# Optimization experiments

Measured on AMD Instinct MI355X. Metric: run time of the kernel, lower is better.

## Reference

```python
import jax, jax.numpy as jnp
import numpy as np
from jax import lax

QMAX = 15.0   # 4-bit unsigned activation levels
BN_EPS = 1e-5


def _binarize_irnet(w):
    # IR-Net style 1-bit weights: per-output-channel normalize, sign, rescale by mean |w|.
    mu = jnp.mean(w, axis=(1, 2, 3), keepdims=True)
    std = jnp.std(w, axis=(1, 2, 3), keepdims=True)
    wn = (w - mu) / (std + 1e-5)
    scale = jnp.mean(jnp.abs(wn), axis=(1, 2, 3), keepdims=True)
    wc = jnp.clip(wn, -1.0, 1.0)
    # STE: forward=sign(wn), backward=hardtanh passthrough
    bw = wc + lax.stop_gradient(jnp.sign(wn) - wc)
    return bw * scale


def _lsq_act_4bit(x, alpha):
    # LSQ unsigned 4-bit: clamp(x/alpha, 0, 15), round with STE, rescale.
    xs = jnp.clip(x / alpha, 0.0, QMAX)
    xq = xs + lax.stop_gradient(jnp.round(xs) - xs)
    return xq * alpha


def _qconv_bn_relu(x, w, alpha, g, b, m, v, stride):
    xq = _lsq_act_4bit(x, alpha)
    bw = _binarize_irnet(w)
    y = lax.conv_general_dilated(
        xq, bw, window_strides=(stride, stride), padding=((1, 1), (1, 1)),
        dimension_numbers=('NCHW', 'OIHW', 'NCHW'))
    inv = g / jnp.sqrt(v + BN_EPS)
    y = y * inv[None, :, None, None] + (b - m * inv)[None, :, None, None]
    return jax.nn.relu(y)


def setup_inputs() -> dict:
    key = jax.random.key(0)
    ks = jax.random.split(key, 3)
    B, C, H, W = 32, 256, 56, 56
    x = jax.random.normal(ks[0], (B, C, H, W), dtype=jnp.float32)
    w1 = jax.random.normal(ks[1], (C, C, 3, 3), dtype=jnp.float32) * 0.05
    w2 = jax.random.normal(ks[2], (C, C, 3, 3), dtype=jnp.float32) * 0.05
    ones = jnp.ones((C,), jnp.float32)
    zeros = jnp.zeros((C,), jnp.float32)
    return {
        'x': x,
        'w1': w1, 'alpha1': jnp.float32(0.1), 'g1': ones, 'b1': zeros, 'm1': zeros, 'v1': ones,
        'w2': w2, 'alpha2': jnp.float32(0.1), 'g2': ones, 'b2': zeros, 'm2': zeros, 'v2': ones,
    }


def reference(x, w1, alpha1, g1, b1, m1, v1, w2, alpha2, g2, b2, m2, v2):
    stride = 1
    h = _qconv_bn_relu(x, w1, alpha1, g1, b1, m1, v1, stride)
    out = _qconv_bn_relu(h, w2, alpha2, g2, b2, m2, v2, 1)
    return out
```

## Files before the change

### kernel.cpp

```cpp
#include <hip/hip_runtime.h>
#include <math.h>

typedef int v4i __attribute__((ext_vector_type(4)));
typedef int v16i __attribute__((ext_vector_type(16)));
typedef unsigned long long u64;

#define Bn 32
#define Cc 256
#define Hh 56
#define Ww 56
#define RSTR (34 * 256)
#define ACT_LDS (6 * RSTR)
#define NSTG (6 * 34 * 16)

__device__ __forceinline__ float block_sum(float v, float* red) {
#pragma unroll
    for (int off = 32; off > 0; off >>= 1) v += __shfl_down(v, off, 64);
    const int wv = threadIdx.x >> 6;
    __syncthreads();
    if ((threadIdx.x & 63) == 0) red[wv] = v;
    __syncthreads();
    return red[0] + red[1] + red[2] + red[3];
}

__global__ __launch_bounds__(256) void k_binpack(const float* __restrict__ w,
                                                 signed char* __restrict__ wf,
                                                 float* __restrict__ wsc) {
    __shared__ float red[4];
    const int o = blockIdx.x;
    const float* wo = w + (size_t)o * 2304;
    const int t = threadIdx.x;
    float v[9];
    float s = 0.f, s2 = 0.f;
#pragma unroll
    for (int i = 0; i < 9; ++i) {
        v[i] = wo[t * 9 + i];
        s += v[i];
        s2 += v[i] * v[i];
    }
    s = block_sum(s, red);
    s2 = block_sum(s2, red);
    const float mu = s * (1.f / 2304.f);
    const float sd = sqrtf(fmaxf(s2 * (1.f / 2304.f) - mu * mu, 0.f));
    float sa = 0.f;
#pragma unroll
    for (int i = 0; i < 9; ++i) sa += fabsf(v[i] - mu);
    sa = block_sum(sa, red);
    if (t == 0) wsc[o] = (sa * (1.f / 2304.f)) / (sd + 1e-5f);
    const int c = t, c32 = c >> 5, hf = (c >> 4) & 1, j = c & 15;
    const int lane = (hf << 5) | (o & 31), octile = o >> 5;
#pragma unroll
    for (int tap = 0; tap < 9; ++tap) {
        const float d = v[tap] - mu;
        const signed char sg = (d > 0.f) ? 1 : ((d < 0.f) ? -1 : 0);
        wf[(size_t)(((tap * 8 + c32) * 8 + octile) * 64 + lane) * 16 + j] = sg;
    }
}

__global__ void k_prep(const float* __restrict__ g1, const float* __restrict__ b1,
                       const float* __restrict__ m1, const float* __restrict__ v1,
                       const float* __restrict__ g2, const float* __restrict__ b2,
                       const float* __restrict__ m2, const float* __restrict__ v2,
                       const float* __restrict__ a1p, const float* __restrict__ a2p,
                       const float* __restrict__ ws1, const float* __restrict__ ws2,
                       float* __restrict__ ep) {
    const int i = threadIdx.x;
    const float i1 = g1[i] / sqrtf(v1[i] + 1e-5f);
    const float i2 = g2[i] / sqrtf(v2[i] + 1e-5f);
    ep[i] = a1p[0] * ws1[i] * i1;
    ep[256 + i] = b1[i] - m1[i] * i1;
    ep[512 + i] = a2p[0] * ws2[i] * i2;
    ep[768 + i] = b2[i] - m2[i] * i2;
}

__global__ __launch_bounds__(256) void k_quant_nhwc(const float* __restrict__ x,
                                                    unsigned char* __restrict__ xq,
                                                    const float* __restrict__ ap) {
    __shared__ unsigned char q[3584];
    const int bid = blockIdx.x;
    const int cg = bid & 3;
    const int h = (bid >> 2) % Hh;
    const int n = bid / (4 * Hh);
    const float a = ap[0];
    const int c0 = cg * 64;
    for (int i = threadIdx.x; i < 3584; i += 256) {
        const int cl = i / 56;
        const int w = i - cl * 56;
        const float v = x[(((size_t)n * Cc + c0 + cl) * Hh + h) * Ww + w];
        const float xs = fminf(fmaxf(v / a, 0.f), 15.f);
        q[w * 64 + (((cl >> 2) ^ (w & 15)) << 2) + (cl & 3)] = (unsigned char)(int)rintf(xs);
    }
    __syncthreads();
    const unsigned int* q32 = (const unsigned int*)q;
    unsigned int* dst = (unsigned int*)xq + ((size_t)(n * Hh + h) * Ww) * 32;
    for (int j = threadIdx.x; j < 448; j += 256) {
        const int w = j >> 3, g8l = (j >> 1) & 3, hf = j & 1;
        const unsigned int lo = q32[w * 16 + ((g8l * 4 + hf) ^ (w & 15))];
        const unsigned int hi = q32[w * 16 + ((g8l * 4 + 2 + hf) ^ (w & 15))];
        dst[w * 32 + (cg * 4 + g8l) * 2 + hf] = lo | (hi << 4);
    }
}

template <bool QOUT>
__global__ __launch_bounds__(256, 3) void k_conv(const unsigned char* __restrict__ xin,
                                                 const signed char* __restrict__ wf,
                                                 const float* __restrict__ ep,
                                                 const float* __restrict__ a2p,
                                                 unsigned char* __restrict__ hq,
                                                 float* __restrict__ yout) {
    __shared__ __align__(16) unsigned char sm[ACT_LDS];
    const int bid = blockIdx.x;
    const int oh = bid & 1;
    const int mh = (bid >> 1) & 1;
    const int hb = (bid >> 2) % 14;
    const int n = (bid >> 2) / 14;
    const int h0 = hb * 4;
    const int mbase = mh * 32;
    const int tid = threadIdx.x;
    const int boff = bid & 7;

    {
        u64 tmp[13];
#pragma unroll
        for (int k = 0; k < 13; ++k) {
            int u = tid + (k << 8);
            u = u > (NSTG - 1) ? (NSTG - 1) : u;
            const int r = u / 544;
            const int rem = u - r * 544;
            const int col = rem >> 4;
            const int t8 = rem & 15;
            int y = h0 - 1 + r;
            int xi = mbase - 1 + col;
            y = y < 0 ? 0 : (y > 55 ? 55 : y);
            xi = xi < 0 ? 0 : (xi > 55 ? 55 : xi);
            tmp[k] = *(const u64*)(xin + ((((size_t)n * Hh + y) * Ww + xi) << 7) + (t8 << 3));
        }
#pragma unroll
        for (int k = 0; k < 13; ++k) {
            const int u = tid + (k << 8);
            if (u < NSTG) {
                const int r = u / 544;
                const int rem = u - r * 544;
                const int col = rem >> 4;
                const int t8 = rem & 15;
                const int y = h0 - 1 + r;
                const int xi = mbase - 1 + col;
                const u64 p = ((unsigned)y < 56u && (unsigned)xi < 56u) ? tmp[k] : 0;
                const u64 lo = p & 0x0F0F0F0F0F0F0F0FULL;
                const u64 hi = (p >> 4) & 0x0F0F0F0F0F0F0F0FULL;
                v4i wv;
                wv[0] = (int)lo;
                wv[1] = (int)(lo >> 32);
                wv[2] = (int)hi;
                wv[3] = (int)(hi >> 32);
                *(v4i*)(sm + r * RSTR + col * 256 + ((t8 ^ (col & 15)) << 4)) = wv;
            }
        }
    }
    __syncthreads();

    const int lane = tid & 63;
    const int g = tid >> 6;
    const int half = lane >> 5;
    const int lm = lane & 31;
    const int octile = oh * 4 + g;

    v16i acc[4] = {};
    const v4i* wpg = (const v4i*)wf + octile * 64 + lane;

    int pkw[3];
#pragma unroll
    for (int kw = 0; kw < 3; ++kw) {
        const int col = lm + kw;
        pkw[kw] = (col * 256) ^ (half << 4) ^ ((col & 15) << 4);
    }

#pragma unroll 1
    for (int ii = 0; ii < 8; ++ii) {
        const int c32 = (ii + boff) & 7;
        v4i aw[9];
#pragma unroll
        for (int tap = 0; tap < 9; ++tap) aw[tap] = wpg[(tap * 8 + c32) << 9];
        const int cs = c32 << 5;
#pragma unroll
        for (int kw = 0; kw < 3; ++kw) {
            const unsigned char* bp = sm + (pkw[kw] ^ cs);
            v4i bfr[6];
#pragma unroll
            for (int ar = 0; ar < 6; ++ar)
                bfr[ar] = *(const v4i*)(bp + ar * RSTR);
#pragma unroll
            for (int kh = 0; kh < 3; ++kh) {
#pragma unroll
                for (int r = 0; r < 4; ++r)
                    acc[r] = __builtin_amdgcn_mfma_i32_32x32x32_i8(aw[kh * 3 + kw],
                                                                   bfr[r + kh], acc[r], 0, 0, 0);
            }
        }
    }

    if constexpr (QOUT) {
        __syncthreads();
        unsigned int* hb = (unsigned int*)sm;
        const float inva = 1.0f / a2p[0];
        const int oc0w = oh * 128 + g * 32;
        const int d0 = 4 * g + half;
#pragma unroll
        for (int r = 0; r < 4; ++r) {
            const v16i av = acc[r];
            unsigned int pk0 = 0, pk1 = 0;
#pragma unroll
            for (int q = 0; q < 4; ++q) {
                const int oc = oc0w + 4 * half + q;
                const unsigned int c0 = (unsigned int)(int)rintf(
                    fminf(fmaxf(fmaf((float)av[q], ep[oc], ep[256 + oc]), 0.f) * inva, 15.f));
                const unsigned int c1 = (unsigned int)(int)rintf(
                    fminf(fmaxf(fmaf((float)av[4 + q], ep[oc + 8], ep[264 + oc]), 0.f) * inva, 15.f));
                const unsigned int c2 = (unsigned int)(int)rintf(
                    fminf(fmaxf(fmaf((float)av[8 + q], ep[oc + 16], ep[272 + oc]), 0.f) * inva, 15.f));
                const unsigned int c3 = (unsigned int)(int)rintf(
                    fminf(fmaxf(fmaf((float)av[12 + q], ep[oc + 24], ep[280 + oc]), 0.f) * inva, 15.f));
                pk0 |= (c0 | (c1 << 4)) << (8 * q);
                pk1 |= (c2 | (c3 << 4)) << (8 * q);
            }
            const int rb = (r * 32 + lm) * 16;
            hb[rb + (d0 ^ (lm & 15))] = pk0;
            hb[rb + ((d0 + 2) ^ (lm & 15))] = pk1;
        }
        __syncthreads();
        unsigned int* dst = (unsigned int*)hq;
        for (int j = tid; j < 4 * 32 * 16; j += 256) {
            const int rw = j >> 4, dw = j & 15;
            const int r = rw >> 5, wl = rw & 31;
            const int w = mbase + wl;
            if (w < 56)
                dst[((size_t)((n * Hh + h0 + r) * Ww) + w) * 32 + oh * 16 + dw] =
                    hb[(rw << 4) + (dw ^ (wl & 15))];
        }
    } else {
        const int w = mbase + lm;
        if (w < 56) {
            float* dst = yout + (size_t)n * Cc * 3136 + (size_t)h0 * 56 + w;
#pragma unroll
            for (int r = 0; r < 4; ++r) {
                const v16i av = acc[r];
#pragma unroll
                for (int reg = 0; reg < 16; ++reg) {
                    const int oc = oh * 128 + g * 32 + (reg & 3) + 8 * (reg >> 2) + 4 * half;
                    dst[(size_t)oc * 3136 + r * 56] =
                        fmaxf(fmaf((float)av[reg], ep[oc], ep[256 + oc]), 0.f);
                }
            }
        }
    }
}

extern "C" void kernel_launch(void* const* d_in, const int* in_sizes, int n_in,
                              void* d_out, int out_size, void* d_ws, size_t ws_size,
                              hipStream_t stream) {
    const float* x = (const float*)d_in[0];
    const float* w1 = (const float*)d_in[1];
    const float* a1 = (const float*)d_in[2];
    const float* g1 = (const float*)d_in[3];
    const float* b1 = (const float*)d_in[4];
    const float* m1 = (const float*)d_in[5];
    const float* v1 = (const float*)d_in[6];
    const float* w2 = (const float*)d_in[7];
    const float* a2 = (const float*)d_in[8];
    const float* g2 = (const float*)d_in[9];
    const float* b2 = (const float*)d_in[10];
    const float* m2 = (const float*)d_in[11];
    const float* v2 = (const float*)d_in[12];

    signed char* wf1 = (signed char*)d_ws;
    signed char* wf2 = wf1 + 589824;
    float* wsc1 = (float*)(wf2 + 589824);
    float* wsc2 = wsc1 + 256;
    float* ep = wsc2 + 256;
    unsigned char* xq1 = (unsigned char*)(ep + 1024);
    unsigned char* hq = xq1 + (size_t)12845056;

    k_binpack<<<256, 256, 0, stream>>>(w1, wf1, wsc1);
    k_binpack<<<256, 256, 0, stream>>>(w2, wf2, wsc2);
    k_prep<<<1, 256, 0, stream>>>(g1, b1, m1, v1, g2, b2, m2, v2, a1, a2, wsc1, wsc2, ep);
    k_quant_nhwc<<<Bn * Hh * 4, 256, 0, stream>>>(x, xq1, a1);

    k_conv<true><<<1792, 256, 0, stream>>>(xq1, wf1, ep, a2, hq, nullptr);
    k_conv<false><<<1792, 256, 0, stream>>>(hq, wf2, ep + 512, nullptr, nullptr, (float*)d_out);
}
```

Baseline: 179.4 us.

## Double-buffer conv MFMA fragments across kernel-column steps and raise MFMA priority

Restructures the inner conv loop into a software pipeline. Weight and activation fragments for the next (kw, channel-chunk) step are loaded into alternate register buffers while the MFMAs for the current step run, which is meant to hide global and LDS load latency behind matrix work. The MFMA bursts are wrapped in s_setprio so that waves holding math get scheduling priority. The channel-chunk start offset is now also staggered per wave, which spreads weight reads across chunks. The cost is more live vector registers under the 3-blocks-per-CU launch bound, which risks lower occupancy or spills, plus one redundant prefetch after the last step.

```diff
diff --git a/kernel.cpp b/kernel.cpp
--- a/kernel.cpp
+++ b/kernel.cpp
@@ -101,6 +101,29 @@
     }
 }
 
+#define LDA(AW, KW, C32)                                                   \
+    do {                                                                   \
+        _Pragma("unroll") for (int kh_ = 0; kh_ < 3; ++kh_)                \
+            AW[kh_] = wpg[((kh_ * 3 + (KW)) * 8 + (C32)) << 9];            \
+    } while (0)
+
+#define LDB(BB, KW, C32)                                                   \
+    do {                                                                   \
+        const unsigned char* bp_ = sm + (pkw[(KW)] ^ ((C32) << 5));        \
+        _Pragma("unroll") for (int ar_ = 0; ar_ < 6; ++ar_)                \
+            BB[ar_] = *(const v4i*)(bp_ + ar_ * RSTR);                     \
+    } while (0)
+
+#define MM(AW, BB)                                                         \
+    do {                                                                   \
+        __builtin_amdgcn_s_setprio(1);                                     \
+        _Pragma("unroll") for (int kh_ = 0; kh_ < 3; ++kh_)                \
+            _Pragma("unroll") for (int r_ = 0; r_ < 4; ++r_)               \
+                acc[r_] = __builtin_amdgcn_mfma_i32_32x32x32_i8(           \
+                    AW[kh_], BB[r_ + kh_], acc[r_], 0, 0, 0);              \
+        __builtin_amdgcn_s_setprio(0);                                     \
+    } while (0)
+
 template <bool QOUT>
 __global__ __launch_bounds__(256, 3) void k_conv(const unsigned char* __restrict__ xin,
                                                  const signed char* __restrict__ wf,
@@ -117,7 +140,6 @@
     const int h0 = hb * 4;
     const int mbase = mh * 32;
     const int tid = threadIdx.x;
-    const int boff = bid & 7;
 
     {
         u64 tmp[13];
@@ -164,6 +186,7 @@
     const int half = lane >> 5;
     const int lm = lane & 31;
     const int octile = oh * 4 + g;
+    const int boff = ((bid << 2) | g) & 7;
 
     v16i acc[4] = {};
     const v4i* wpg = (const v4i*)wf + octile * 64 + lane;
@@ -175,28 +198,22 @@
         pkw[kw] = (col * 256) ^ (half << 4) ^ ((col & 15) << 4);
     }
 
+    v4i awA[3], awB[3], bA[6], bB[6];
+    LDA(awA, 0, boff);
+    LDB(bA, 0, boff);
+
 #pragma unroll 1
-    for (int ii = 0; ii < 8; ++ii) {
-        const int c32 = (ii + boff) & 7;
-        v4i aw[9];
-#pragma unroll
-        for (int tap = 0; tap < 9; ++tap) aw[tap] = wpg[(tap * 8 + c32) << 9];
-        const int cs = c32 << 5;
-#pragma unroll
-        for (int kw = 0; kw < 3; ++kw) {
-            const unsigned char* bp = sm + (pkw[kw] ^ cs);
-            v4i bfr[6];
-#pragma unroll
-            for (int ar = 0; ar < 6; ++ar)
-                bfr[ar] = *(const v4i*)(bp + ar * RSTR);
-#pragma unroll
-            for (int kh = 0; kh < 3; ++kh) {
-#pragma unroll
-                for (int r = 0; r < 4; ++r)
-                    acc[r] = __builtin_amdgcn_mfma_i32_32x32x32_i8(aw[kh * 3 + kw],
-                                                                   bfr[r + kh], acc[r], 0, 0, 0);
-            }
-        }
+    for (int s6 = 0; s6 < 24; s6 += 6) {
+        const int i0 = s6 / 3;
+        const int ca = (i0 + boff) & 7;
+        const int cb = (i0 + 1 + boff) & 7;
+        const int cc = (i0 + 2 + boff) & 7;
+        LDA(awB, 1, ca); LDB(bB, 1, ca); MM(awA, bA);
+        LDA(awA, 2, ca); LDB(bA, 2, ca); MM(awB, bB);
+        LDA(awB, 0, cb); LDB(bB, 0, cb); MM(awA, bA);
+        LDA(awA, 1, cb); LDB(bA, 1, cb); MM(awB, bB);
+        LDA(awB, 2, cb); LDB(bB, 2, cb); MM(awA, bA);
+        LDA(awA, 0, cc); LDB(bA, 0, cc); MM(awB, bB);
     }
 
     if constexpr (QOUT) {
```

New measurement: 173.8 us. 1.03x faster.

## Compute all 256 output channels per block to halve activation tile staging

Applied to the files above, without the earlier changes.

Each conv block now covers all 256 output channels, with each wave handling two 32-channel tiles, instead of splitting channels across two blocks. This halves the grid and removes the duplicated LDS staging of the activation halo tile, and each LDS B-fragment now feeds twice as many MFMAs. Weight loads are moved inside the kw loop, and the MFMA burst is wrapped in s_setprio. The cost is twice the accumulator registers, with launch bounds lowered from 3 to 2 blocks per CU, and fewer blocks to spread across CUs.

```diff
diff --git a/kernel.cpp b/kernel.cpp
--- a/kernel.cpp
+++ b/kernel.cpp
@@ -102,7 +102,7 @@
 }
 
 template <bool QOUT>
-__global__ __launch_bounds__(256, 3) void k_conv(const unsigned char* __restrict__ xin,
+__global__ __launch_bounds__(256, 2) void k_conv(const unsigned char* __restrict__ xin,
                                                  const signed char* __restrict__ wf,
                                                  const float* __restrict__ ep,
                                                  const float* __restrict__ a2p,
@@ -110,14 +110,12 @@
                                                  float* __restrict__ yout) {
     __shared__ __align__(16) unsigned char sm[ACT_LDS];
     const int bid = blockIdx.x;
-    const int oh = bid & 1;
-    const int mh = (bid >> 1) & 1;
-    const int hb = (bid >> 2) % 14;
-    const int n = (bid >> 2) / 14;
+    const int mh = bid & 1;
+    const int hb = (bid >> 1) % 14;
+    const int n = (bid >> 1) / 14;
     const int h0 = hb * 4;
     const int mbase = mh * 32;
     const int tid = threadIdx.x;
-    const int boff = bid & 7;
 
     {
         u64 tmp[13];
@@ -163,10 +161,10 @@
     const int g = tid >> 6;
     const int half = lane >> 5;
     const int lm = lane & 31;
-    const int octile = oh * 4 + g;
-
-    v16i acc[4] = {};
-    const v4i* wpg = (const v4i*)wf + octile * 64 + lane;
+    const int boff = ((bid << 2) | g) & 7;
+
+    v16i acc[2][4] = {};
+    const v4i* wpg = (const v4i*)wf + (2 * g) * 64 + lane;
 
     int pkw[3];
 #pragma unroll
@@ -178,9 +176,6 @@
 #pragma unroll 1
     for (int ii = 0; ii < 8; ++ii) {
         const int c32 = (ii + boff) & 7;
-        v4i aw[9];
-#pragma unroll
-        for (int tap = 0; tap < 9; ++tap) aw[tap] = wpg[(tap * 8 + c32) << 9];
         const int cs = c32 << 5;
 #pragma unroll
         for (int kw = 0; kw < 3; ++kw) {
@@ -189,13 +184,24 @@
 #pragma unroll
             for (int ar = 0; ar < 6; ++ar)
                 bfr[ar] = *(const v4i*)(bp + ar * RSTR);
+            v4i aw0[3], aw1[3];
 #pragma unroll
             for (int kh = 0; kh < 3; ++kh) {
-#pragma unroll
-                for (int r = 0; r < 4; ++r)
-                    acc[r] = __builtin_amdgcn_mfma_i32_32x32x32_i8(aw[kh * 3 + kw],
-                                                                   bfr[r + kh], acc[r], 0, 0, 0);
+                const int idx = ((kh * 3 + kw) * 8 + c32) << 9;
+                aw0[kh] = wpg[idx];
+                aw1[kh] = wpg[idx + 64];
             }
+            __builtin_amdgcn_s_setprio(1);
+#pragma unroll
+            for (int kh = 0; kh < 3; ++kh)
+#pragma unroll
+                for (int r = 0; r < 4; ++r) {
+                    acc[0][r] = __builtin_amdgcn_mfma_i32_32x32x32_i8(aw0[kh], bfr[r + kh],
+                                                                      acc[0][r], 0, 0, 0);
+                    acc[1][r] = __builtin_amdgcn_mfma_i32_32x32x32_i8(aw1[kh], bfr[r + kh],
+                                                                      acc[1][r], 0, 0, 0);
+                }
+            __builtin_amdgcn_s_setprio(0);
         }
     }
 
@@ -203,54 +209,60 @@
         __syncthreads();
         unsigned int* hb = (unsigned int*)sm;
         const float inva = 1.0f / a2p[0];
-        const int oc0w = oh * 128 + g * 32;
-        const int d0 = 4 * g + half;
-#pragma unroll
-        for (int r = 0; r < 4; ++r) {
-            const v16i av = acc[r];
-            unsigned int pk0 = 0, pk1 = 0;
-#pragma unroll
-            for (int q = 0; q < 4; ++q) {
-                const int oc = oc0w + 4 * half + q;
-                const unsigned int c0 = (unsigned int)(int)rintf(
-                    fminf(fmaxf(fmaf((float)av[q], ep[oc], ep[256 + oc]), 0.f) * inva, 15.f));
-                const unsigned int c1 = (unsigned int)(int)rintf(
-                    fminf(fmaxf(fmaf((float)av[4 + q], ep[oc + 8], ep[264 + oc]), 0.f) * inva, 15.f));
-                const unsigned int c2 = (unsigned int)(int)rintf(
-                    fminf(fmaxf(fmaf((float)av[8 + q], ep[oc + 16], ep[272 + oc]), 0.f) * inva, 15.f));
-                const unsigned int c3 = (unsigned int)(int)rintf(
-                    fminf(fmaxf(fmaf((float)av[12 + q], ep[oc + 24], ep[280 + oc]), 0.f) * inva, 15.f));
-                pk0 |= (c0 | (c1 << 4)) << (8 * q);
-                pk1 |= (c2 | (c3 << 4)) << (8 * q);
+#pragma unroll
+        for (int oct = 0; oct < 2; ++oct) {
+            const int ocb = g * 64 + oct * 32;
+            const int d0 = 8 * g + 4 * oct + half;
+#pragma unroll
+            for (int r = 0; r < 4; ++r) {
+                const v16i av = acc[oct][r];
+                unsigned int pk0 = 0, pk1 = 0;
+#pragma unroll
+                for (int q = 0; q < 4; ++q) {
+                    const int oc = ocb + 4 * half + q;
+                    const unsigned int c0 = (unsigned int)(int)rintf(
+                        fminf(fmaxf(fmaf((float)av[q], ep[oc], ep[256 + oc]), 0.f) * inva, 15.f));
+                    const unsigned int c1 = (unsigned int)(int)rintf(
+                        fminf(fmaxf(fmaf((float)av[4 + q], ep[oc + 8], ep[264 + oc]), 0.f) * inva, 15.f));
+                    const unsigned int c2 = (unsigned int)(int)rintf(
+                        fminf(fmaxf(fmaf((float)av[8 + q], ep[oc + 16], ep[272 + oc]), 0.f) * inva, 15.f));
+                    const unsigned int c3 = (unsigned int)(int)rintf(
+                        fminf(fmaxf(fmaf((float)av[12 + q], ep[oc + 24], ep[280 + oc]), 0.f) * inva, 15.f));
+                    pk0 |= (c0 | (c1 << 4)) << (8 * q);
+                    pk1 |= (c2 | (c3 << 4)) << (8 * q);
+                }
+                const int rb = (r * 32 + lm) * 32;
+                hb[rb + (d0 ^ lm)] = pk0;
+                hb[rb + ((d0 + 2) ^ lm)] = pk1;
             }
-            const int rb = (r * 32 + lm) * 16;
-            hb[rb + (d0 ^ (lm & 15))] = pk0;
-            hb[rb + ((d0 + 2) ^ (lm & 15))] = pk1;
         }
         __syncthreads();
         unsigned int* dst = (unsigned int*)hq;
-        for (int j = tid; j < 4 * 32 * 16; j += 256) {
-            const int rw = j >> 4, dw = j & 15;
-            const int r = rw >> 5, wl = rw & 31;
+        for (int j = tid; j < 4 * 32 * 32; j += 256) {
+            const int dw = j & 31;
+            const int wl = (j >> 5) & 31;
+            const int r = j >> 10;
             const int w = mbase + wl;
             if (w < 56)
-                dst[((size_t)((n * Hh + h0 + r) * Ww) + w) * 32 + oh * 16 + dw] =
-                    hb[(rw << 4) + (dw ^ (wl & 15))];
+                dst[((size_t)((n * Hh + h0 + r) * Ww) + w) * 32 + dw] =
+                    hb[((r * 32 + wl) << 5) + (dw ^ wl)];
         }
     } else {
         const int w = mbase + lm;
         if (w < 56) {
             float* dst = yout + (size_t)n * Cc * 3136 + (size_t)h0 * 56 + w;
 #pragma unroll
-            for (int r = 0; r < 4; ++r) {
-                const v16i av = acc[r];
-#pragma unroll
-                for (int reg = 0; reg < 16; ++reg) {
-                    const int oc = oh * 128 + g * 32 + (reg & 3) + 8 * (reg >> 2) + 4 * half;
-                    dst[(size_t)oc * 3136 + r * 56] =
-                        fmaxf(fmaf((float)av[reg], ep[oc], ep[256 + oc]), 0.f);
+            for (int oct = 0; oct < 2; ++oct)
+#pragma unroll
+                for (int r = 0; r < 4; ++r) {
+                    const v16i av = acc[oct][r];
+#pragma unroll
+                    for (int reg = 0; reg < 16; ++reg) {
+                        const int oc = g * 64 + oct * 32 + (reg & 3) + 8 * (reg >> 2) + 4 * half;
+                        dst[(size_t)oc * 3136 + r * 56] =
+                            fmaxf(fmaf((float)av[reg], ep[oc], ep[256 + oc]), 0.f);
+                    }
                 }
-            }
         }
     }
 }
@@ -285,6 +297,6 @@
     k_prep<<<1, 256, 0, stream>>>(g1, b1, m1, v1, g2, b2, m2, v2, a1, a2, wsc1, wsc2, ep);
     k_quant_nhwc<<<Bn * Hh * 4, 256, 0, stream>>>(x, xq1, a1);
 
-    k_conv<true><<<1792, 256, 0, stream>>>(xq1, wf1, ep, a2, hq, nullptr);
-    k_conv<false><<<1792, 256, 0, stream>>>(hq, wf2, ep + 512, nullptr, nullptr, (float*)d_out);
-}
+    k_conv<true><<<896, 256, 0, stream>>>(xq1, wf1, ep, a2, hq, nullptr);
+    k_conv<false><<<896, 256, 0, stream>>>(hq, wf2, ep + 512, nullptr, nullptr, (float*)d_out);
+}
```

Result: slower. 194.0 us (+8.1%).

## Split MFMA accumulators into two chains and interleave per-kw weight loads with setprio

Applied to the files above, without the earlier changes.

Splits the four accumulators into two alternating sets (accA/accB) so back-to-back MFMAs never depend on the previous result. Weight fragments are now loaded per kw group, 3 at a time instead of 9, and each MFMA burst is wrapped in s_setprio. The per-wave channel-block rotation now also includes the wave index, which staggers LDS and global access. Doubling the accumulator registers forces launch bounds down from 3 to 2 blocks per CU, trading occupancy for more instruction-level parallelism in the MFMA chain.

```diff
diff --git a/kernel.cpp b/kernel.cpp
--- a/kernel.cpp
+++ b/kernel.cpp
@@ -101,8 +101,31 @@
     }
 }
 
+#define KWG(II, KW, X, Y, Z)                                                  \
+    do {                                                                      \
+        const int c32_ = ((II) + boff) & 7;                                   \
+        const unsigned char* bp_ = sm + (pkw[(KW)] ^ (c32_ << 5));            \
+        v4i bfr_[6];                                                          \
+        _Pragma("unroll") for (int ar_ = 0; ar_ < 6; ++ar_)                   \
+            bfr_[ar_] = *(const v4i*)(bp_ + ar_ * RSTR);                      \
+        v4i aw_[3];                                                           \
+        _Pragma("unroll") for (int kh_ = 0; kh_ < 3; ++kh_)                   \
+            aw_[kh_] = wpg[((kh_ * 3 + (KW)) * 8 + c32_) << 9];               \
+        __builtin_amdgcn_s_setprio(1);                                        \
+        _Pragma("unroll") for (int r_ = 0; r_ < 4; ++r_)                      \
+            X[r_] = __builtin_amdgcn_mfma_i32_32x32x32_i8(aw_[0], bfr_[r_],   \
+                                                          X[r_], 0, 0, 0);    \
+        _Pragma("unroll") for (int r_ = 0; r_ < 4; ++r_)                      \
+            Y[r_] = __builtin_amdgcn_mfma_i32_32x32x32_i8(aw_[1], bfr_[r_ + 1],\
+                                                          Y[r_], 0, 0, 0);    \
+        _Pragma("unroll") for (int r_ = 0; r_ < 4; ++r_)                      \
+            Z[r_] = __builtin_amdgcn_mfma_i32_32x32x32_i8(aw_[2], bfr_[r_ + 2],\
+                                                          Z[r_], 0, 0, 0);    \
+        __builtin_amdgcn_s_setprio(0);                                        \
+    } while (0)
+
 template <bool QOUT>
-__global__ __launch_bounds__(256, 3) void k_conv(const unsigned char* __restrict__ xin,
+__global__ __launch_bounds__(256, 2) void k_conv(const unsigned char* __restrict__ xin,
                                                  const signed char* __restrict__ wf,
                                                  const float* __restrict__ ep,
                                                  const float* __restrict__ a2p,
@@ -117,7 +140,6 @@
     const int h0 = hb * 4;
     const int mbase = mh * 32;
     const int tid = threadIdx.x;
-    const int boff = bid & 7;
 
     {
         u64 tmp[13];
@@ -164,8 +186,9 @@
     const int half = lane >> 5;
     const int lm = lane & 31;
     const int octile = oh * 4 + g;
-
-    v16i acc[4] = {};
+    const int boff = ((bid << 2) | g) & 7;
+
+    v16i accA[4] = {}, accB[4] = {};
     const v4i* wpg = (const v4i*)wf + octile * 64 + lane;
 
     int pkw[3];
@@ -176,27 +199,14 @@
     }
 
 #pragma unroll 1
-    for (int ii = 0; ii < 8; ++ii) {
-        const int c32 = (ii + boff) & 7;
-        v4i aw[9];
-#pragma unroll
-        for (int tap = 0; tap < 9; ++tap) aw[tap] = wpg[(tap * 8 + c32) << 9];
-        const int cs = c32 << 5;
-#pragma unroll
-        for (int kw = 0; kw < 3; ++kw) {
-            const unsigned char* bp = sm + (pkw[kw] ^ cs);
-            v4i bfr[6];
-#pragma unroll
-            for (int ar = 0; ar < 6; ++ar)
-                bfr[ar] = *(const v4i*)(bp + ar * RSTR);
-#pragma unroll
-            for (int kh = 0; kh < 3; ++kh) {
-#pragma unroll
-                for (int r = 0; r < 4; ++r)
-                    acc[r] = __builtin_amdgcn_mfma_i32_32x32x32_i8(aw[kh * 3 + kw],
-                                                                   bfr[r + kh], acc[r], 0, 0, 0);
-            }
-        }
+    for (int ip = 0; ip < 4; ++ip) {
+        const int i0 = ip * 2;
+        KWG(i0, 0, accA, accB, accA);
+        KWG(i0, 1, accB, accA, accB);
+        KWG(i0, 2, accA, accB, accA);
+        KWG(i0 + 1, 0, accB, accA, accB);
+        KWG(i0 + 1, 1, accA, accB, accA);
+        KWG(i0 + 1, 2, accB, accA, accB);
     }
 
     if constexpr (QOUT) {
@@ -207,7 +217,7 @@
         const int d0 = 4 * g + half;
 #pragma unroll
         for (int r = 0; r < 4; ++r) {
-            const v16i av = acc[r];
+            const v16i av = accA[r] + accB[r];
             unsigned int pk0 = 0, pk1 = 0;
 #pragma unroll
             for (int q = 0; q < 4; ++q) {
@@ -243,7 +253,7 @@
             float* dst = yout + (size_t)n * Cc * 3136 + (size_t)h0 * 56 + w;
 #pragma unroll
             for (int r = 0; r < 4; ++r) {
-                const v16i av = acc[r];
+                const v16i av = accA[r] + accB[r];
 #pragma unroll
                 for (int reg = 0; reg < 16; ++reg) {
                     const int oc = oh * 128 + g * 32 + (reg & 3) + 8 * (reg >> 2) + 4 * half;
```

Measured after the change: 190.6 us. 1.06x slower.
